# Kernel optimization log

Hardware: AMD Instinct MI355X
Metric: run time of the kernel (lower is better)

The kernel has to match this reference:

```python
import jax, jax.numpy as jnp
import numpy as np

NDIM = 8
P = NDIM * (NDIM - 1) // 2  # 28 upper-triangular pairs
NHIDDEN = 128
NLAYERS = 3  # first layer + (NLAYERS-1) hidden layers, all followed by softplus
BATCH = 65536


def _pair_indices():
    # torch code iterates j outer, i inner, keeping i < j (i >= j skipped)
    pairs = [(i, j) for j in range(NDIM) for i in range(NDIM) if i < j]
    rel = np.array([[k for k in range(NDIM) if k != i and k != j] for (i, j) in pairs],
                   dtype=np.int32)  # [P, NDIM-2]
    i_idx = np.array([p[0] for p in pairs], dtype=np.int32)
    j_idx = np.array([p[1] for p in pairs], dtype=np.int32)
    return rel, i_idx, j_idx


def setup_inputs() -> dict:
    key = jax.random.key(0)
    ks = jax.random.split(key, 7)
    rel, i_idx, j_idx = _pair_indices()
    d_in = NDIM - 2
    x = jax.random.normal(ks[0], (BATCH, NDIM), dtype=jnp.float32)
    # stacked per-pair MLP parameters (kaiming-ish scale)
    W1 = jax.random.normal(ks[1], (P, d_in, NHIDDEN), dtype=jnp.float32) / np.sqrt(d_in)
    b1 = jax.random.normal(ks[2], (P, NHIDDEN), dtype=jnp.float32) * 0.05
    Wh = jax.random.normal(ks[3], (NLAYERS - 1, P, NHIDDEN, NHIDDEN), dtype=jnp.float32) / np.sqrt(NHIDDEN)
    bh = jax.random.normal(ks[4], (NLAYERS - 1, P, NHIDDEN), dtype=jnp.float32) * 0.05
    Wout = jax.random.normal(ks[5], (P, NHIDDEN), dtype=jnp.float32) / np.sqrt(NHIDDEN)
    bout = jax.random.normal(ks[6], (P,), dtype=jnp.float32) * 0.05
    return {
        "x": x, "W1": W1, "b1": b1, "Wh": Wh, "bh": bh,
        "Wout": Wout, "bout": bout,
        "rel_idx": jnp.asarray(rel), "i_idx": jnp.asarray(i_idx), "j_idx": jnp.asarray(j_idx),
    }


def reference(x, W1, b1, Wh, bh, Wout, bout, rel_idx, i_idx, j_idx):
    # gather the ndim-2 relevant coords for every pair: [B, P, NDIM-2]
    xg = x[:, rel_idx]
    # first linear + softplus (batched over the P pairs)
    h = jax.nn.softplus(jnp.einsum('bpd,pdh->bph', xg, W1) + b1)
    # hidden linears + softplus
    for l in range(Wh.shape[0]):
        h = jax.nn.softplus(jnp.einsum('bph,phk->bpk', h, Wh[l]) + bh[l])
    # output head (no activation): scalar per pair -> [B, P]
    vals = jnp.einsum('bph,ph->bp', h, Wout) + bout
    # scatter into upper triangle, then antisymmetrize
    B = x.shape[0]
    J = jnp.zeros((B, NDIM, NDIM), dtype=x.dtype).at[:, i_idx, j_idx].set(vals)
    return J - jnp.swapaxes(J, 1, 2)
```

## Files before the change

### kernel.cpp

```cpp
#include <hip/hip_runtime.h>

#define NDIM 8
#define P_PAIRS 28
#define HID 128
#define BATCH_N 65536
#define TILE_M 256
#define THREADS 1024
#define TILES_PER_BLOCK 4

#define LOG2E 1.4426950408889634f
#define LN2   0.6931471805599453f

typedef __attribute__((ext_vector_type(8))) short bf16x8;
typedef __attribute__((ext_vector_type(4))) float f32x4;

#define MEM_FENCE asm volatile("" ::: "memory")

__device__ __forceinline__ unsigned short f32_to_bf16(float f) {
  union { float f; unsigned u; } v; v.f = f;
  unsigned r = v.u + 0x7FFFu + ((v.u >> 16) & 1u);
  return (unsigned short)(r >> 16);
}

__device__ __forceinline__ unsigned cvt_pk_bf16(float a, float b) {
  unsigned r;
  asm("v_cvt_pk_bf16_f32 %0, %1, %2" : "=v"(r) : "v"(a), "v"(b));
  return r;
}

__device__ __forceinline__ float fast_exp2(float x) {
  float r; asm("v_exp_f32 %0, %1" : "=v"(r) : "v"(x)); return r;
}
__device__ __forceinline__ float fast_log2(float x) {
  float r; asm("v_log_f32 %0, %1" : "=v"(r) : "v"(x)); return r;
}

__device__ __forceinline__ float softplus2(float t) {
  t = fminf(t, 30.0f);
  return fast_log2(1.0f + fast_exp2(t));
}

__device__ __forceinline__ int swz(int r, int c8) {
  return r * 128 + (((c8 ^ (r & 15)) & 15) << 3);
}

__global__ void prep_wt(const float* __restrict__ Wh, unsigned short* __restrict__ WT) {
  __shared__ float tile[32][33];
  int t = blockIdx.x;
  int lp = t >> 4;
  int sub = t & 15;
  int kt = (sub >> 2) * 32, nt = (sub & 3) * 32;
  const float* src = Wh + (size_t)lp * 16384;
  unsigned short* dst = WT + (size_t)lp * 16384;
  int tx = threadIdx.x & 31, ty = threadIdx.x >> 5;
#pragma unroll
  for (int r = 0; r < 32; r += 8)
    tile[r + ty][tx] = src[(kt + r + ty) * 128 + (nt + tx)];
  __syncthreads();
#pragma unroll
  for (int r = 0; r < 32; r += 8)
    dst[(nt + r + ty) * 128 + (kt + tx)] = f32_to_bf16(tile[tx][r + ty]);
}

__launch_bounds__(THREADS, 4)
__global__ void mlp_pairs(const float* __restrict__ x,
                          const float* __restrict__ W1,
                          const float* __restrict__ b1,
                          const float* __restrict__ bh,
                          const float* __restrict__ Wout,
                          const float* __restrict__ bout,
                          const int* __restrict__ rel_idx,
                          const int* __restrict__ i_idx,
                          const int* __restrict__ j_idx,
                          const unsigned short* __restrict__ WT,
                          float* __restrict__ out) {
  const int p = blockIdx.y;
  const int bx = blockIdx.x;
  const int tid = (int)threadIdx.x;
  const int lane = tid & 63;
  const int wave = tid >> 6;
  const int qd = lane >> 4;
  const int ln = lane & 15;
  const int mrow = wave * 16;

  __shared__ __align__(16) unsigned short w0_lds[128 * 128];
  __shared__ __align__(16) unsigned short w1_lds[128 * 128];
  __shared__ __align__(16) unsigned short h_lds[TILE_M * 128];
  __shared__ __align__(16) unsigned short w1t_lds[128][8];
  __shared__ __align__(16) float bh0s[128];
  __shared__ __align__(16) float bh1s[128];
  __shared__ __align__(16) float wouts[128];

  {
    const uint4* s0 = reinterpret_cast<const uint4*>(WT + (size_t)p * 16384);
    const uint4* s1 = reinterpret_cast<const uint4*>(WT + (size_t)(P_PAIRS + p) * 16384);
#pragma unroll
    for (int it = 0; it < 2; ++it) {
      int idx = it * THREADS + tid;
      int r = idx >> 4, c = idx & 15;
      uint4 a = s0[idx];
      uint4 b = s1[idx];
      int off = swz(r, c);
      *reinterpret_cast<uint4*>(&w0_lds[off]) = a;
      *reinterpret_cast<uint4*>(&w1_lds[off]) = b;
    }
  }
  const int ii = i_idx[p], jj = j_idx[p];
  if (tid < 128) {
    int n = tid;
    unsigned short u[8];
#pragma unroll
    for (int k = 0; k < 8; ++k) {
      int d = k - (k > ii) - (k > jj);
      float w;
      if (k == ii)      w = b1[p * 128 + n] * LOG2E;
      else if (k == jj) w = 0.f;
      else              w = W1[(p * 6 + d) * 128 + n] * LOG2E;
      u[k] = f32_to_bf16(w);
    }
    uint4 pk;
    pk.x = (unsigned)u[0] | ((unsigned)u[1] << 16);
    pk.y = (unsigned)u[2] | ((unsigned)u[3] << 16);
    pk.z = (unsigned)u[4] | ((unsigned)u[5] << 16);
    pk.w = (unsigned)u[6] | ((unsigned)u[7] << 16);
    *reinterpret_cast<uint4*>(&w1t_lds[n][0]) = pk;
  } else if (tid < 256) {
    int n = tid - 128;
    bh0s[n] = bh[p * 128 + n] * LOG2E;
    bh1s[n] = bh[(P_PAIRS + p) * 128 + n] * LOG2E;
    wouts[n] = Wout[p * 128 + n] * LN2;
  }
  const float bp = bout[p];

  unsigned amsk[4], omsk[4];
  {
    unsigned am = (ii & 1) ? 0x0000FFFFu : 0xFFFF0000u;
    unsigned om = 0x3F80u << ((ii & 1) * 16);
    int wi = ii >> 1;
#pragma unroll
    for (int w = 0; w < 4; ++w) {
      amsk[w] = (w == wi) ? am : 0xFFFFFFFFu;
      omsk[w] = (w == wi) ? om : 0u;
    }
  }
  __syncthreads();

  const int phase = wave >> 2;

  const int ln3 = ln & 3;
  const int rdx = ((qd ^ ln3) << 3) + ((ln >> 2) << 5);
  const int a0  = ln * 128 + rdx;
  const int b0  = (mrow + ln) * 128 + rdx;
  const int hw0 = (mrow + ln) * 128 + (((qd >> 1) ^ (ln & 1)) << 3)
                + (((ln >> 1) & 7) << 4) + (qd & 1) * 4;

  f32x4 wreg[8];
#pragma unroll
  for (int nt = 0; nt < 8; ++nt)
    wreg[nt] = *reinterpret_cast<const f32x4*>(&wouts[nt * 16 + qd * 4]);

  float4 xa = {0.f, 0.f, 0.f, 0.f}, xb = {0.f, 0.f, 0.f, 0.f};
  {
    int row = bx * (TILE_M * TILES_PER_BLOCK) + phase * TILE_M + mrow + ln;
    const float4* xr = reinterpret_cast<const float4*>(x + (size_t)row * 8);
    if (lane < 16) { xa = xr[0]; xb = xr[1]; }
  }

  for (int s = 0; s < TILES_PER_BLOCK; ++s) {
    const int itile = (s + phase) & 3;
    const int row0 = bx * (TILE_M * TILES_PER_BLOCK) + itile * TILE_M;

    bf16x8 zero8 = {};
    bf16x8 bfr1 = zero8;
    if (lane < 16) {
      uint4 pk;
      pk.x = (cvt_pk_bf16(xa.x, xa.y) & amsk[0]) | omsk[0];
      pk.y = (cvt_pk_bf16(xa.z, xa.w) & amsk[1]) | omsk[1];
      pk.z = (cvt_pk_bf16(xb.x, xb.y) & amsk[2]) | omsk[2];
      pk.w = (cvt_pk_bf16(xb.z, xb.w) & amsk[3]) | omsk[3];
      bfr1 = __builtin_bit_cast(bf16x8, pk);
    }
    if (s + 1 < TILES_PER_BLOCK && lane < 16) {
      int nrow0 = bx * (TILE_M * TILES_PER_BLOCK) + (((s + 1 + phase) & 3)) * TILE_M;
      const float4* xr = reinterpret_cast<const float4*>(x + (size_t)(nrow0 + mrow + ln) * 8);
      xa = xr[0]; xb = xr[1];
    }

    f32x4 acc[8];

    {
      f32x4 zc = {0.f, 0.f, 0.f, 0.f};
#pragma unroll
      for (int nt = 0; nt < 8; ++nt) {
        bf16x8 afr = zero8;
        if (qd == 0)
          afr = *reinterpret_cast<const bf16x8*>(&w1t_lds[nt * 16 + ln][0]);
        acc[nt] = __builtin_amdgcn_mfma_f32_16x16x32_bf16(afr, bfr1, zc, 0, 0, 0);
      }
    }
#pragma unroll
    for (int nt = 0; nt < 8; ++nt) {
      uint2 pk;
      pk.x = cvt_pk_bf16(softplus2(acc[nt][0]), softplus2(acc[nt][1]));
      pk.y = cvt_pk_bf16(softplus2(acc[nt][2]), softplus2(acc[nt][3]));
      *reinterpret_cast<uint2*>(&h_lds[hw0 ^ (nt << 4)]) = pk;
    }
    MEM_FENCE;

    {
      bf16x8 bfr = *reinterpret_cast<const bf16x8*>(&h_lds[b0]);
#pragma unroll
      for (int nt = 0; nt < 8; ++nt) {
        bf16x8 afr = *reinterpret_cast<const bf16x8*>(&w0_lds[a0 + nt * 2048]);
        f32x4 b4 = *reinterpret_cast<const f32x4*>(&bh0s[nt * 16 + qd * 4]);
        acc[nt] = __builtin_amdgcn_mfma_f32_16x16x32_bf16(afr, bfr, b4, 0, 0, 0);
      }
    }
#pragma unroll
    for (int ks = 1; ks < 4; ++ks) {
      bf16x8 bfr = *reinterpret_cast<const bf16x8*>(&h_lds[b0 ^ (ks << 5)]);
      bf16x8 afr[8];
#pragma unroll
      for (int nt = 0; nt < 8; ++nt)
        afr[nt] = *reinterpret_cast<const bf16x8*>(&w0_lds[(a0 ^ (ks << 5)) + nt * 2048]);
#pragma unroll
      for (int nt = 0; nt < 8; ++nt)
        acc[nt] = __builtin_amdgcn_mfma_f32_16x16x32_bf16(afr[nt], bfr, acc[nt], 0, 0, 0);
    }
#pragma unroll
    for (int nt = 0; nt < 8; ++nt) {
      uint2 pk;
      pk.x = cvt_pk_bf16(softplus2(acc[nt][0]), softplus2(acc[nt][1]));
      pk.y = cvt_pk_bf16(softplus2(acc[nt][2]), softplus2(acc[nt][3]));
      *reinterpret_cast<uint2*>(&h_lds[hw0 ^ (nt << 4)]) = pk;
    }
    MEM_FENCE;

    {
      bf16x8 bfr = *reinterpret_cast<const bf16x8*>(&h_lds[b0]);
#pragma unroll
      for (int nt = 0; nt < 8; ++nt) {
        bf16x8 afr = *reinterpret_cast<const bf16x8*>(&w1_lds[a0 + nt * 2048]);
        f32x4 b4 = *reinterpret_cast<const f32x4*>(&bh1s[nt * 16 + qd * 4]);
        acc[nt] = __builtin_amdgcn_mfma_f32_16x16x32_bf16(afr, bfr, b4, 0, 0, 0);
      }
    }
#pragma unroll
    for (int ks = 1; ks < 4; ++ks) {
      bf16x8 bfr = *reinterpret_cast<const bf16x8*>(&h_lds[b0 ^ (ks << 5)]);
      bf16x8 afr[8];
#pragma unroll
      for (int nt = 0; nt < 8; ++nt)
        afr[nt] = *reinterpret_cast<const bf16x8*>(&w1_lds[(a0 ^ (ks << 5)) + nt * 2048]);
#pragma unroll
      for (int nt = 0; nt < 8; ++nt)
        acc[nt] = __builtin_amdgcn_mfma_f32_16x16x32_bf16(afr[nt], bfr, acc[nt], 0, 0, 0);
    }
    float pv = 0.f;
#pragma unroll
    for (int nt = 0; nt < 8; ++nt) {
#pragma unroll
      for (int r = 0; r < 4; ++r)
        pv += wreg[nt][r] * softplus2(acc[nt][r]);
    }

    {
      float v = pv;
      v += __shfl_xor(v, 16, 64);
      v += __shfl_xor(v, 32, 64);
      if (lane < 16) {
        int mg = row0 + mrow + lane;
        float val = v + bp;
        out[mg * 64 + ii * 8 + jj] = val;
        out[mg * 64 + jj * 8 + ii] = -val;
        if (p == 0) {
#pragma unroll
          for (int d = 0; d < 8; ++d)
            out[mg * 64 + d * 9] = 0.f;
        }
      }
    }
    MEM_FENCE;
  }
}

extern "C" void kernel_launch(void* const* d_in, const int* in_sizes, int n_in,
                              void* d_out, int out_size, void* d_ws, size_t ws_size,
                              hipStream_t stream) {
  const float* x    = (const float*)d_in[0];
  const float* W1   = (const float*)d_in[1];
  const float* b1   = (const float*)d_in[2];
  const float* Wh   = (const float*)d_in[3];
  const float* bh   = (const float*)d_in[4];
  const float* Wout = (const float*)d_in[5];
  const float* bout = (const float*)d_in[6];
  const int* rel    = (const int*)d_in[7];
  const int* iidx   = (const int*)d_in[8];
  const int* jidx   = (const int*)d_in[9];
  float* out = (float*)d_out;
  unsigned short* WT = (unsigned short*)d_ws;

  prep_wt<<<dim3(56 * 16), 256, 0, stream>>>(Wh, WT);
  dim3 grid(BATCH_N / (TILE_M * TILES_PER_BLOCK), P_PAIRS);
  mlp_pairs<<<grid, THREADS, 0, stream>>>(x, W1, b1, bh, Wout, bout, rel, iidx, jidx, WT, out);
}
```

Baseline: 308.4 us.

## Keep hidden activations in registers via permlane swaps instead of LDS round-trip

```diff
diff --git a/kernel.cpp b/kernel.cpp
--- a/kernel.cpp
+++ b/kernel.cpp
@@ -13,8 +13,6 @@
 
 typedef __attribute__((ext_vector_type(8))) short bf16x8;
 typedef __attribute__((ext_vector_type(4))) float f32x4;
-
-#define MEM_FENCE asm volatile("" ::: "memory")
 
 __device__ __forceinline__ unsigned short f32_to_bf16(float f) {
   union { float f; unsigned u; } v; v.f = f;
@@ -85,7 +83,6 @@
 
   __shared__ __align__(16) unsigned short w0_lds[128 * 128];
   __shared__ __align__(16) unsigned short w1_lds[128 * 128];
-  __shared__ __align__(16) unsigned short h_lds[TILE_M * 128];
   __shared__ __align__(16) unsigned short w1t_lds[128][8];
   __shared__ __align__(16) float bh0s[128];
   __shared__ __align__(16) float bh1s[128];
@@ -150,9 +147,6 @@
   const int ln3 = ln & 3;
   const int rdx = ((qd ^ ln3) << 3) + ((ln >> 2) << 5);
   const int a0  = ln * 128 + rdx;
-  const int b0  = (mrow + ln) * 128 + rdx;
-  const int hw0 = (mrow + ln) * 128 + (((qd >> 1) ^ (ln & 1)) << 3)
-                + (((ln >> 1) & 7) << 4) + (qd & 1) * 4;
 
   f32x4 wreg[8];
 #pragma unroll
@@ -198,63 +192,73 @@
         acc[nt] = __builtin_amdgcn_mfma_f32_16x16x32_bf16(afr, bfr1, zc, 0, 0, 0);
       }
     }
-#pragma unroll
-    for (int nt = 0; nt < 8; ++nt) {
-      uint2 pk;
-      pk.x = cvt_pk_bf16(softplus2(acc[nt][0]), softplus2(acc[nt][1]));
-      pk.y = cvt_pk_bf16(softplus2(acc[nt][2]), softplus2(acc[nt][3]));
-      *reinterpret_cast<uint2*>(&h_lds[hw0 ^ (nt << 4)]) = pk;
-    }
-    MEM_FENCE;
+
+    bf16x8 bfr2[4];
+#pragma unroll
+    for (int ks = 0; ks < 4; ++ks) {
+      unsigned A = cvt_pk_bf16(softplus2(acc[2*ks][0]),   softplus2(acc[2*ks][1]));
+      unsigned B = cvt_pk_bf16(softplus2(acc[2*ks][2]),   softplus2(acc[2*ks][3]));
+      unsigned C = cvt_pk_bf16(softplus2(acc[2*ks+1][0]), softplus2(acc[2*ks+1][1]));
+      unsigned D = cvt_pk_bf16(softplus2(acc[2*ks+1][2]), softplus2(acc[2*ks+1][3]));
+      asm("v_permlane32_swap_b32 %0, %1" : "+v"(A), "+v"(C));
+      asm("v_permlane32_swap_b32 %0, %1" : "+v"(B), "+v"(D));
+      asm("v_permlane16_swap_b32 %0, %1" : "+v"(A), "+v"(C));
+      asm("v_permlane16_swap_b32 %0, %1" : "+v"(B), "+v"(D));
+      uint4 g; g.x = A; g.y = B; g.z = C; g.w = D;
+      bfr2[ks] = __builtin_bit_cast(bf16x8, g);
+    }
 
     {
-      bf16x8 bfr = *reinterpret_cast<const bf16x8*>(&h_lds[b0]);
 #pragma unroll
       for (int nt = 0; nt < 8; ++nt) {
         bf16x8 afr = *reinterpret_cast<const bf16x8*>(&w0_lds[a0 + nt * 2048]);
         f32x4 b4 = *reinterpret_cast<const f32x4*>(&bh0s[nt * 16 + qd * 4]);
-        acc[nt] = __builtin_amdgcn_mfma_f32_16x16x32_bf16(afr, bfr, b4, 0, 0, 0);
+        acc[nt] = __builtin_amdgcn_mfma_f32_16x16x32_bf16(afr, bfr2[0], b4, 0, 0, 0);
       }
     }
 #pragma unroll
     for (int ks = 1; ks < 4; ++ks) {
-      bf16x8 bfr = *reinterpret_cast<const bf16x8*>(&h_lds[b0 ^ (ks << 5)]);
       bf16x8 afr[8];
 #pragma unroll
       for (int nt = 0; nt < 8; ++nt)
         afr[nt] = *reinterpret_cast<const bf16x8*>(&w0_lds[(a0 ^ (ks << 5)) + nt * 2048]);
 #pragma unroll
       for (int nt = 0; nt < 8; ++nt)
-        acc[nt] = __builtin_amdgcn_mfma_f32_16x16x32_bf16(afr[nt], bfr, acc[nt], 0, 0, 0);
-    }
-#pragma unroll
-    for (int nt = 0; nt < 8; ++nt) {
-      uint2 pk;
-      pk.x = cvt_pk_bf16(softplus2(acc[nt][0]), softplus2(acc[nt][1]));
-      pk.y = cvt_pk_bf16(softplus2(acc[nt][2]), softplus2(acc[nt][3]));
-      *reinterpret_cast<uint2*>(&h_lds[hw0 ^ (nt << 4)]) = pk;
-    }
-    MEM_FENCE;
+        acc[nt] = __builtin_amdgcn_mfma_f32_16x16x32_bf16(afr[nt], bfr2[ks], acc[nt], 0, 0, 0);
+    }
+
+    bf16x8 bfr3[4];
+#pragma unroll
+    for (int ks = 0; ks < 4; ++ks) {
+      unsigned A = cvt_pk_bf16(softplus2(acc[2*ks][0]),   softplus2(acc[2*ks][1]));
+      unsigned B = cvt_pk_bf16(softplus2(acc[2*ks][2]),   softplus2(acc[2*ks][3]));
+      unsigned C = cvt_pk_bf16(softplus2(acc[2*ks+1][0]), softplus2(acc[2*ks+1][1]));
+      unsigned D = cvt_pk_bf16(softplus2(acc[2*ks+1][2]), softplus2(acc[2*ks+1][3]));
+      asm("v_permlane32_swap_b32 %0, %1" : "+v"(A), "+v"(C));
+      asm("v_permlane32_swap_b32 %0, %1" : "+v"(B), "+v"(D));
+      asm("v_permlane16_swap_b32 %0, %1" : "+v"(A), "+v"(C));
+      asm("v_permlane16_swap_b32 %0, %1" : "+v"(B), "+v"(D));
+      uint4 g; g.x = A; g.y = B; g.z = C; g.w = D;
+      bfr3[ks] = __builtin_bit_cast(bf16x8, g);
+    }
 
     {
-      bf16x8 bfr = *reinterpret_cast<const bf16x8*>(&h_lds[b0]);
 #pragma unroll
       for (int nt = 0; nt < 8; ++nt) {
         bf16x8 afr = *reinterpret_cast<const bf16x8*>(&w1_lds[a0 + nt * 2048]);
         f32x4 b4 = *reinterpret_cast<const f32x4*>(&bh1s[nt * 16 + qd * 4]);
-        acc[nt] = __builtin_amdgcn_mfma_f32_16x16x32_bf16(afr, bfr, b4, 0, 0, 0);
+        acc[nt] = __builtin_amdgcn_mfma_f32_16x16x32_bf16(afr, bfr3[0], b4, 0, 0, 0);
       }
     }
 #pragma unroll
     for (int ks = 1; ks < 4; ++ks) {
-      bf16x8 bfr = *reinterpret_cast<const bf16x8*>(&h_lds[b0 ^ (ks << 5)]);
       bf16x8 afr[8];
 #pragma unroll
       for (int nt = 0; nt < 8; ++nt)
         afr[nt] = *reinterpret_cast<const bf16x8*>(&w1_lds[(a0 ^ (ks << 5)) + nt * 2048]);
 #pragma unroll
       for (int nt = 0; nt < 8; ++nt)
-        acc[nt] = __builtin_amdgcn_mfma_f32_16x16x32_bf16(afr[nt], bfr, acc[nt], 0, 0, 0);
+        acc[nt] = __builtin_amdgcn_mfma_f32_16x16x32_bf16(afr[nt], bfr3[ks], acc[nt], 0, 0, 0);
     }
     float pv = 0.f;
 #pragma unroll
@@ -280,7 +284,6 @@
         }
       }
     }
-    MEM_FENCE;
   }
 }
 
```

New measurement: 329.7 us. 6.9% more time.
